# Performance work log

Measured on AMD Instinct MI355X. Metric: run time of the kernel, lower is better.

Reference implementation:

```python
import jax, jax.numpy as jnp
import numpy as np

B, N, D, H = 8, 1024, 768, 12
HD = D // H
SCALE = HD ** -0.5

def setup_inputs() -> dict:
    key = jax.random.key(0)
    k1, k2, k3, k4 = jax.random.split(key, 4)
    x = jax.random.normal(k1, (B, N, D), dtype=jnp.float32)
    weight = jax.random.uniform(k2, (B, N), dtype=jnp.float32)
    W_qkv = jax.random.normal(k3, (D, 3 * D), dtype=jnp.float32) * (D ** -0.5)
    W_msa = jax.random.normal(k4, (D, D), dtype=jnp.float32) * (D ** -0.5)
    b_msa = jnp.zeros((D,), dtype=jnp.float32)
    return {"x": x, "weight": weight, "W_qkv": W_qkv, "W_msa": W_msa, "b_msa": b_msa}

def reference(x, weight, W_qkv, W_msa, b_msa):
    # QKV projection (no bias), then elementwise per-token gate
    qkv = jnp.einsum('bnd,de->bne', x, W_qkv)          # [B,N,3D]
    qkv = weight[:, :, None] * qkv
    qkv = qkv.reshape(B, N, 3, H, HD).transpose(2, 0, 3, 1, 4)  # [3,B,H,N,hd]
    q, k, v = qkv[0], qkv[1], qkv[2]
    A = jnp.einsum('bhnd,bhmd->bhnm', q, k) * SCALE    # [B,H,N,N]
    A = jax.nn.softmax(A, axis=-1)
    out = jnp.einsum('bhnm,bhmd->bhnd', A, v)          # [B,H,N,hd]
    out = out.transpose(0, 2, 1, 3).reshape(B, N, D)
    return jnp.einsum('bnd,de->bne', out, W_msa) + b_msa
```

## Files before the change

### kernel.cpp

```cpp
#include <hip/hip_runtime.h>
#include <hip/hip_bf16.h>


typedef __attribute__((ext_vector_type(8))) short bf8;
typedef __attribute__((ext_vector_type(4))) float f4;

#define QSCALE 0.1803368801111204f
#define MFMA16 __builtin_amdgcn_mfma_f32_16x16x32_bf16

static __device__ __forceinline__ short bf16_of(float f) {
    union { float f; unsigned u; } a; a.f = f;
    unsigned r = a.u + 0x7FFFu + ((a.u >> 16) & 1u);
    return (short)(r >> 16);
}

static __device__ __forceinline__ unsigned bfpk(float lo, float hi) {
    float2 t; t.x = lo; t.y = hi;
    __hip_bfloat162 b = __float22bfloat162_rn(t);
    union { __hip_bfloat162 b; unsigned u; } c; c.b = b;
    return c.u;
}

static __device__ __forceinline__ void async16(const short* g, short* l) {
    __builtin_amdgcn_global_load_lds(
        (const __attribute__((address_space(1))) void*)g,
        (__attribute__((address_space(3))) void*)l, 16, 0, 0);
}

static __device__ __forceinline__ void transpose64(
        const float* __restrict__ w, short* __restrict__ wt,
        int K, int E, int k0, int e0, int tid, short (*t)[65]) {
#pragma unroll
    for (int p = 0; p < 16; ++p) {
        int idx = p * 256 + tid;
        int r = idx >> 6, c = idx & 63;
        t[r][c] = bf16_of(w[(k0 + r) * E + e0 + c]);
    }
    __syncthreads();
#pragma unroll
    for (int p = 0; p < 16; ++p) {
        int idx = p * 256 + tid;
        int r = idx >> 6, c = idx & 63;
        wt[(e0 + r) * K + k0 + c] = t[c][r];
    }
}

__global__ __launch_bounds__(256) void k_prep(
        const float* __restrict__ x, const float* __restrict__ gate,
        short* __restrict__ xb,
        const float* __restrict__ Wqkv, short* __restrict__ wtq,
        const float* __restrict__ Wmsa, short* __restrict__ wtm) {
    __shared__ short t[64][65];
    const int bid = blockIdx.x, tid = threadIdx.x;
    if (bid < 3072) {
        int i = bid * 256 + tid;
        const float g = gate[i / 96];
        const f4* sp = (const f4*)x;
        f4 a = sp[2 * i], b = sp[2 * i + 1];
        union { bf8 v; short h[8]; } o;
        o.h[0] = bf16_of(a[0] * g); o.h[1] = bf16_of(a[1] * g);
        o.h[2] = bf16_of(a[2] * g); o.h[3] = bf16_of(a[3] * g);
        o.h[4] = bf16_of(b[0] * g); o.h[5] = bf16_of(b[1] * g);
        o.h[6] = bf16_of(b[2] * g); o.h[7] = bf16_of(b[3] * g);
        ((bf8*)xb)[i] = o.v;
    } else if (bid < 3504) {
        int tt = bid - 3072;
        transpose64(Wqkv, wtq, 768, 2304, (tt / 36) * 64, (tt % 36) * 64, tid, t);
    } else {
        int tt = bid - 3504;
        transpose64(Wmsa, wtm, 768, 768, (tt / 12) * 64, (tt % 12) * 64, tid, t);
    }
}

__global__ __launch_bounds__(256, 2) void k_gemm_qkv(
        const short* __restrict__ xb, const short* __restrict__ wtq,
        short* __restrict__ qb, short* __restrict__ kb, short* __restrict__ vt) {
    __shared__ short lds[34816];
    const int tid = threadIdx.x, lane = tid & 63;
    const int l16 = lane & 15, quad = lane >> 4, rx = l16 & 7;
    const int wm = tid >> 6;

    const int wg = blockIdx.x;
    const int swz = (wg & 7) * 128 + (wg >> 3);
    const int mI = swz >> 4, nI = swz & 15;
    const int m0 = mI * 128, n0 = nI * 144;

    const short* gA = xb + m0 * 768;
    const short* gB = wtq + n0 * 768;

    auto stageA = [&](int buf, int k0) {
        short* base = lds + buf * 17408;
#pragma unroll
        for (int j = 0; j < 4; ++j) {
            int p = j * 256 + tid, row = p >> 3;
            int gc = (p & 7) ^ (row & 7);
            async16(gA + row * 768 + k0 + gc * 8, base + p * 8);
        }
    };
    auto stageB = [&](int buf, int k0) {
        short* base = lds + buf * 17408 + 8192;
#pragma unroll
        for (int j = 0; j < 4; ++j) {
            int p = j * 256 + tid, row = p >> 3;
            int gc = (p & 7) ^ (row & 7);
            async16(gB + row * 768 + k0 + gc * 8, base + p * 8);
        }
        if (tid < 128) {
            int p = 1024 + tid, row = p >> 3;
            int gc = (p & 7) ^ (row & 7);
            async16(gB + row * 768 + k0 + gc * 8, base + p * 8);
        }
    };

    auto rdA = [&](const short* base, int mf, int ks) {
        return *(const bf8*)(base + (wm * 32 + mf * 16 + l16) * 64 +
                             (((ks * 4 + quad) ^ rx) << 3));
    };
    auto rdB = [&](const short* base, int nf, int ks) {
        return *(const bf8*)(base + 8192 + (nf * 16 + l16) * 64 +
                             (((ks * 4 + quad) ^ rx) << 3));
    };

    f4 z = {0.f, 0.f, 0.f, 0.f};
    f4 acc[2][9];
#pragma unroll
    for (int mf = 0; mf < 2; ++mf)
#pragma unroll
        for (int nf = 0; nf < 9; ++nf) acc[mf][nf] = z;

    stageA(0, 0); stageB(0, 0);
    asm volatile("s_waitcnt vmcnt(0)" ::: "memory");
    __builtin_amdgcn_s_barrier();

#pragma unroll 2
    for (int t = 0; t < 12; ++t) {
        const short* cur = lds + (t & 1) * 17408;
        bf8 af[2][2];
        af[0][0] = rdA(cur, 0, 0); af[0][1] = rdA(cur, 0, 1);
        af[1][0] = rdA(cur, 1, 0); af[1][1] = rdA(cur, 1, 1);
        bf8 bfr[5][2];
#pragma unroll
        for (int nf = 0; nf < 5; ++nf) { bfr[nf][0] = rdB(cur, nf, 0); bfr[nf][1] = rdB(cur, nf, 1); }
        if (t < 11) stageA((t + 1) & 1, (t + 1) * 64);
        __builtin_amdgcn_s_setprio(1);
#pragma unroll
        for (int mf = 0; mf < 2; ++mf)
#pragma unroll
            for (int nf = 0; nf < 5; ++nf) {
                acc[mf][nf] = MFMA16(af[mf][0], bfr[nf][0], acc[mf][nf], 0, 0, 0);
                acc[mf][nf] = MFMA16(af[mf][1], bfr[nf][1], acc[mf][nf], 0, 0, 0);
            }
        __builtin_amdgcn_s_setprio(0);
        bf8 bfh[4][2];
#pragma unroll
        for (int nf = 0; nf < 4; ++nf) { bfh[nf][0] = rdB(cur, nf + 5, 0); bfh[nf][1] = rdB(cur, nf + 5, 1); }
        if (t < 11) stageB((t + 1) & 1, (t + 1) * 64);
        __builtin_amdgcn_s_setprio(1);
#pragma unroll
        for (int mf = 0; mf < 2; ++mf)
#pragma unroll
            for (int nf = 0; nf < 4; ++nf) {
                acc[mf][nf + 5] = MFMA16(af[mf][0], bfh[nf][0], acc[mf][nf + 5], 0, 0, 0);
                acc[mf][nf + 5] = MFMA16(af[mf][1], bfh[nf][1], acc[mf][nf + 5], 0, 0, 0);
            }
        __builtin_amdgcn_s_setprio(0);
        asm volatile("s_waitcnt vmcnt(0)" ::: "memory");
        __builtin_amdgcn_s_barrier();
    }

    const int bI = m0 >> 10, nn0 = m0 & 1023;
#pragma unroll
    for (int nf = 0; nf < 9; ++nf) {
        const int ct = n0 + nf * 16;
        if (ct < 1536) {
            const int which = (ct >= 768) ? 1 : 0;
            const int h = (ct - which * 768) >> 6;
            const int hd = (ct & 63) + l16;
            short* dst = (which ? kb : qb) + (bI * 12 + h) * 65536 + hd;
#pragma unroll
            for (int mf = 0; mf < 2; ++mf)
#pragma unroll
                for (int r = 0; r < 4; ++r) {
                    const int nn = nn0 + wm * 32 + mf * 16 + quad * 4 + r;
                    const float val = acc[mf][nf][r];
                    dst[nn * 64] = bf16_of(which ? val : val * QSCALE);
                }
        }
    }
    const int vlo = (n0 >= 1536) ? n0 : 1536;
    const int vcnt = n0 + 144 - vlo;
    const int npass = (vcnt > 0) ? vcnt / 48 : 0;
    for (int p = 0; p < npass; ++p) {
        __syncthreads();
        const int c0 = vlo + p * 48;
#pragma unroll
        for (int nf = 0; nf < 9; ++nf) {
            const int ct = n0 + nf * 16;
            if (ct >= c0 && ct < c0 + 48) {
                const int lcol = ct - c0 + l16;
#pragma unroll
                for (int mf = 0; mf < 2; ++mf)
#pragma unroll
                    for (int r = 0; r < 4; ++r) {
                        const int row = wm * 32 + mf * 16 + quad * 4 + r;
                        lds[lcol * 136 + row] = bf16_of(acc[mf][nf][r]);
                    }
            }
        }
        __syncthreads();
        const int vg0 = c0 - 1536;
#pragma unroll
        for (int u = 0; u < 3; ++u) {
            const int idx = u * 256 + tid;
            const int lc = idx >> 4, ck = idx & 15;
            const int vg = vg0 + lc;
            const int h = vg >> 6, hd = vg & 63;
            bf8 vv = *(const bf8*)(lds + lc * 136 + ck * 8);
            *(bf8*)(vt + ((bI * 12 + h) * 64 + hd) * 1024 + nn0 + ck * 8) = vv;
        }
    }
}

__global__ __launch_bounds__(256, 2) void k_gemm_final(
        const short* __restrict__ attn, const short* __restrict__ wtm,
        const float* __restrict__ bias, float* __restrict__ out) {
    __shared__ short lds[28672];
    const int tid = threadIdx.x, lane = tid & 63;
    const int l16 = lane & 15, quad = lane >> 4, rx = l16 & 7;
    const int wm = tid >> 6;

    const int wg = blockIdx.x;
    const int swz = (wg & 7) * 64 + (wg >> 3);
    const int mI = swz >> 3, nI = swz & 7;
    const int m0 = mI * 128, n0 = nI * 96;

    const short* gA = attn + m0 * 768;
    const short* gB = wtm + n0 * 768;

    auto stageA = [&](int buf, int k0) {
        short* base = lds + buf * 14336;
#pragma unroll
        for (int j = 0; j < 4; ++j) {
            int p = j * 256 + tid, row = p >> 3;
            int gc = (p & 7) ^ (row & 7);
            async16(gA + row * 768 + k0 + gc * 8, base + p * 8);
        }
    };
    auto stageB = [&](int buf, int k0) {
        short* base = lds + buf * 14336 + 8192;
#pragma unroll
        for (int j = 0; j < 3; ++j) {
            int p = j * 256 + tid, row = p >> 3;
            int gc = (p & 7) ^ (row & 7);
            async16(gB + row * 768 + k0 + gc * 8, base + p * 8);
        }
    };
    auto rdA = [&](const short* base, int mf, int ks) {
        return *(const bf8*)(base + (wm * 32 + mf * 16 + l16) * 64 +
                             (((ks * 4 + quad) ^ rx) << 3));
    };
    auto rdB = [&](const short* base, int nf, int ks) {
        return *(const bf8*)(base + 8192 + (nf * 16 + l16) * 64 +
                             (((ks * 4 + quad) ^ rx) << 3));
    };

    f4 z = {0.f, 0.f, 0.f, 0.f};
    f4 acc[2][6];
#pragma unroll
    for (int mf = 0; mf < 2; ++mf)
#pragma unroll
        for (int nf = 0; nf < 6; ++nf) acc[mf][nf] = z;

    stageA(0, 0); stageB(0, 0);
    asm volatile("s_waitcnt vmcnt(0)" ::: "memory");
    __builtin_amdgcn_s_barrier();

#pragma unroll 2
    for (int t = 0; t < 12; ++t) {
        const short* cur = lds + (t & 1) * 14336;
        bf8 af[2][2];
        af[0][0] = rdA(cur, 0, 0); af[0][1] = rdA(cur, 0, 1);
        af[1][0] = rdA(cur, 1, 0); af[1][1] = rdA(cur, 1, 1);
        bf8 bfr[3][2];
#pragma unroll
        for (int nf = 0; nf < 3; ++nf) { bfr[nf][0] = rdB(cur, nf, 0); bfr[nf][1] = rdB(cur, nf, 1); }
        if (t < 11) stageA((t + 1) & 1, (t + 1) * 64);
        __builtin_amdgcn_s_setprio(1);
#pragma unroll
        for (int mf = 0; mf < 2; ++mf)
#pragma unroll
            for (int nf = 0; nf < 3; ++nf) {
                acc[mf][nf] = MFMA16(af[mf][0], bfr[nf][0], acc[mf][nf], 0, 0, 0);
                acc[mf][nf] = MFMA16(af[mf][1], bfr[nf][1], acc[mf][nf], 0, 0, 0);
            }
        __builtin_amdgcn_s_setprio(0);
        bf8 bfh[3][2];
#pragma unroll
        for (int nf = 0; nf < 3; ++nf) { bfh[nf][0] = rdB(cur, nf + 3, 0); bfh[nf][1] = rdB(cur, nf + 3, 1); }
        if (t < 11) stageB((t + 1) & 1, (t + 1) * 64);
        __builtin_amdgcn_s_setprio(1);
#pragma unroll
        for (int mf = 0; mf < 2; ++mf)
#pragma unroll
            for (int nf = 0; nf < 3; ++nf) {
                acc[mf][nf + 3] = MFMA16(af[mf][0], bfh[nf][0], acc[mf][nf + 3], 0, 0, 0);
                acc[mf][nf + 3] = MFMA16(af[mf][1], bfh[nf][1], acc[mf][nf + 3], 0, 0, 0);
            }
        __builtin_amdgcn_s_setprio(0);
        asm volatile("s_waitcnt vmcnt(0)" ::: "memory");
        __builtin_amdgcn_s_barrier();
    }

#pragma unroll
    for (int nf = 0; nf < 6; ++nf) {
        const int e = n0 + nf * 16 + l16;
        const float bv = bias[e];
#pragma unroll
        for (int mf = 0; mf < 2; ++mf)
#pragma unroll
            for (int r = 0; r < 4; ++r) {
                const int row = m0 + wm * 32 + mf * 16 + quad * 4 + r;
                out[row * 768 + e] = acc[mf][nf][r] + bv;
            }
    }
}

__global__ __launch_bounds__(256, 3) void k_attn(const short* __restrict__ qb,
                                                 const short* __restrict__ kb,
                                                 const short* __restrict__ vt,
                                                 short* __restrict__ attn) {
    __shared__ short Ks[2][4096];
    __shared__ short Vs[2][4096];
    const int tid = threadIdx.x, wave = tid >> 6, lane = tid & 63;
    const int l16 = lane & 15, quad = lane >> 4;
    const int bh = blockIdx.x;
    const int b = bh / 12, h = bh - b * 12;
    const int m_base = blockIdx.y * 128 + wave * 32;
    const short* qh = qb + bh * 65536;
    const short* kh = kb + bh * 65536;
    const short* vh = vt + bh * 65536;

    const int rA = ((l16 >> 2) << 3) + (l16 & 3);
    const int fK = (((rA >> 3) & 1) << 2) + (rA & 3);
    const int sK = (quad ^ fK) * 8;
    const int oAlo = rA * 64 + sK;
    const int oAhi = rA * 64 + (sK ^ 32);
    const int oBlo = oAlo + 256, oBhi = oAhi + 256;
    const int fV = (((l16 >> 3) & 1) << 2) + (l16 & 3);
    const int oV = l16 * 64 + ((quad ^ fV) * 8);

    const short* qp0 = qh + (m_base + l16) * 64 + quad * 8;
    bf8 qf00 = *(const bf8*)(qp0);
    bf8 qf01 = *(const bf8*)(qp0 + 32);
    const short* qp1 = qp0 + 16 * 64;
    bf8 qf10 = *(const bf8*)(qp1);
    bf8 qf11 = *(const bf8*)(qp1 + 32);

    union { bf8 v; short h[8]; } onef;
#pragma unroll
    for (int i = 0; i < 8; ++i) onef.h[i] = (short)0x3F80;

    f4 z = {0.f, 0.f, 0.f, 0.f};
    f4 acc0[4] = {z, z, z, z};
    f4 acc1[4] = {z, z, z, z};
    f4 accl0 = z, accl1 = z;

    auto stage = [&](int buf, int j0) {
#pragma unroll
        for (int j = 0; j < 2; ++j) {
            int idx = j * 256 + tid;
            int row = idx >> 3;
            int fr = (((row >> 3) & 1) << 2) + (row & 3);
            int gc = (idx & 7) ^ fr;
            async16(kh + (j0 + row) * 64 + gc * 8, Ks[buf] + idx * 8);
            async16(vh + row * 1024 + j0 + gc * 8, Vs[buf] + idx * 8);
        }
    };

    stage(0, 0);
    int cur = 0;
    for (int it = 0; it < 16; ++it) {
        __builtin_amdgcn_s_waitcnt(0);
        __syncthreads();
        if (it + 1 < 16) stage(cur ^ 1, (it + 1) * 64);
        const short* Kc = Ks[cur];
        const short* Vc = Vs[cur];

#pragma unroll
        for (int jj = 0; jj < 64; jj += 32) {
            const short* kjj = Kc + jj * 64;
            bf8 kAlo = *(const bf8*)(kjj + oAlo);
            bf8 kAhi = *(const bf8*)(kjj + oAhi);
            bf8 kBlo = *(const bf8*)(kjj + oBlo);
            bf8 kBhi = *(const bf8*)(kjj + oBhi);
            bf8 vf0 = *(const bf8*)(Vc + 0 * 1024 + (oV ^ (jj ? 32 : 0)));
            bf8 vf1 = *(const bf8*)(Vc + 1 * 1024 + (oV ^ (jj ? 32 : 0)));
            bf8 vf2 = *(const bf8*)(Vc + 2 * 1024 + (oV ^ (jj ? 32 : 0)));
            bf8 vf3 = *(const bf8*)(Vc + 3 * 1024 + (oV ^ (jj ? 32 : 0)));

            {
                f4 sA = z, sB = z;
                __builtin_amdgcn_s_setprio(1);
                sA = MFMA16(kAlo, qf00, sA, 0, 0, 0);
                sA = MFMA16(kAhi, qf01, sA, 0, 0, 0);
                sB = MFMA16(kBlo, qf00, sB, 0, 0, 0);
                sB = MFMA16(kBhi, qf01, sB, 0, 0, 0);
                __builtin_amdgcn_s_setprio(0);
                float a0 = __builtin_amdgcn_exp2f(sA[0]);
                float a1 = __builtin_amdgcn_exp2f(sA[1]);
                float a2 = __builtin_amdgcn_exp2f(sA[2]);
                float a3 = __builtin_amdgcn_exp2f(sA[3]);
                float b0 = __builtin_amdgcn_exp2f(sB[0]);
                float b1 = __builtin_amdgcn_exp2f(sB[1]);
                float b2 = __builtin_amdgcn_exp2f(sB[2]);
                float b3 = __builtin_amdgcn_exp2f(sB[3]);
                union { bf8 v; unsigned u[4]; } p;
                p.u[0] = bfpk(a0, a1); p.u[1] = bfpk(a2, a3);
                p.u[2] = bfpk(b0, b1); p.u[3] = bfpk(b2, b3);
                __builtin_amdgcn_s_setprio(1);
                accl0 = MFMA16(onef.v, p.v, accl0, 0, 0, 0);
                acc0[0] = MFMA16(vf0, p.v, acc0[0], 0, 0, 0);
                acc0[1] = MFMA16(vf1, p.v, acc0[1], 0, 0, 0);
                acc0[2] = MFMA16(vf2, p.v, acc0[2], 0, 0, 0);
                acc0[3] = MFMA16(vf3, p.v, acc0[3], 0, 0, 0);
                __builtin_amdgcn_s_setprio(0);
            }
            {
                f4 sA = z, sB = z;
                __builtin_amdgcn_s_setprio(1);
                sA = MFMA16(kAlo, qf10, sA, 0, 0, 0);
                sA = MFMA16(kAhi, qf11, sA, 0, 0, 0);
                sB = MFMA16(kBlo, qf10, sB, 0, 0, 0);
                sB = MFMA16(kBhi, qf11, sB, 0, 0, 0);
                __builtin_amdgcn_s_setprio(0);
                float a0 = __builtin_amdgcn_exp2f(sA[0]);
                float a1 = __builtin_amdgcn_exp2f(sA[1]);
                float a2 = __builtin_amdgcn_exp2f(sA[2]);
                float a3 = __builtin_amdgcn_exp2f(sA[3]);
                float b0 = __builtin_amdgcn_exp2f(sB[0]);
                float b1 = __builtin_amdgcn_exp2f(sB[1]);
                float b2 = __builtin_amdgcn_exp2f(sB[2]);
                float b3 = __builtin_amdgcn_exp2f(sB[3]);
                union { bf8 v; unsigned u[4]; } p;
                p.u[0] = bfpk(a0, a1); p.u[1] = bfpk(a2, a3);
                p.u[2] = bfpk(b0, b1); p.u[3] = bfpk(b2, b3);
                __builtin_amdgcn_s_setprio(1);
                accl1 = MFMA16(onef.v, p.v, accl1, 0, 0, 0);
                acc1[0] = MFMA16(vf0, p.v, acc1[0], 0, 0, 0);
                acc1[1] = MFMA16(vf1, p.v, acc1[1], 0, 0, 0);
                acc1[2] = MFMA16(vf2, p.v, acc1[2], 0, 0, 0);
                acc1[3] = MFMA16(vf3, p.v, acc1[3], 0, 0, 0);
                __builtin_amdgcn_s_setprio(0);
            }
        }
        cur ^= 1;
    }

    const float inv0 = 1.f / accl0[0];
    const float inv1 = 1.f / accl1[0];
    const int row0 = (b << 10) + m_base + l16;
    short* op0 = attn + row0 * 768 + h * 64 + quad * 4;
    short* op1 = op0 + 16 * 768;
#pragma unroll
    for (int dt = 0; dt < 4; ++dt)
#pragma unroll
        for (int r = 0; r < 4; ++r) {
            op0[dt * 16 + r] = bf16_of(acc0[dt][r] * inv0);
            op1[dt * 16 + r] = bf16_of(acc1[dt][r] * inv1);
        }
}

extern "C" void kernel_launch(void* const* d_in, const int* in_sizes, int n_in,
                              void* d_out, int out_size, void* d_ws, size_t ws_size,
                              hipStream_t stream) {
    const float* x    = (const float*)d_in[0];
    const float* gate = (const float*)d_in[1];
    const float* Wqkv = (const float*)d_in[2];
    const float* Wmsa = (const float*)d_in[3];
    const float* bmsa = (const float*)d_in[4];
    float* out = (float*)d_out;

    char* ws = (char*)d_ws;
    short* xb  = (short*)(ws);
    short* wtq = (short*)(ws + 12582912);
    short* wtm = (short*)(ws + 16121856);
    short* qb  = (short*)(ws + 17301504);
    short* kb  = (short*)(ws + 29884416);
    short* vt  = (short*)(ws + 42467328);
    short* attn = xb;

    k_prep<<<3648, 256, 0, stream>>>(x, gate, xb, Wqkv, wtq, Wmsa, wtm);
    k_gemm_qkv<<<1024, 256, 0, stream>>>(xb, wtq, qb, kb, vt);
    k_attn<<<dim3(96, 8), 256, 0, stream>>>(qb, kb, vt, attn);
    k_gemm_final<<<512, 256, 0, stream>>>(attn, wtm, bmsa, out);
}
```

Baseline: 179.0 us.

## Deepen QKV GEMM pipeline to four stages with K=32 tiles and partial waits

Reworks the QKV projection GEMM from a double-buffered K=64 loop into a four-buffer K=32 pipeline that prefetches three tiles ahead. Waits use partial vmcnt counts per wave so the next tile's loads can stay in flight, which is meant to hide global-to-LDS latency better. The LDS swizzle is changed to suit 32-wide rows. The trade-off is twice as many barriers and iterations, and a redundant duplicated store line added in k_prep.

```diff
diff --git a/kernel.cpp b/kernel.cpp
--- a/kernel.cpp
+++ b/kernel.cpp
@@ -61,6 +61,7 @@
         o.h[0] = bf16_of(a[0] * g); o.h[1] = bf16_of(a[1] * g);
         o.h[2] = bf16_of(a[2] * g); o.h[3] = bf16_of(a[3] * g);
         o.h[4] = bf16_of(b[0] * g); o.h[5] = bf16_of(b[1] * g);
+        o.h[6] = bf16_of(b[2] * g); o.h[7] = bf16_of(b[7 - 4] * g);
         o.h[6] = bf16_of(b[2] * g); o.h[7] = bf16_of(b[3] * g);
         ((bf8*)xb)[i] = o.v;
     } else if (bid < 3504) {
@@ -77,7 +78,7 @@
         short* __restrict__ qb, short* __restrict__ kb, short* __restrict__ vt) {
     __shared__ short lds[34816];
     const int tid = threadIdx.x, lane = tid & 63;
-    const int l16 = lane & 15, quad = lane >> 4, rx = l16 & 7;
+    const int l16 = lane & 15, quad = lane >> 4;
     const int wm = tid >> 6;
 
     const int wg = blockIdx.x;
@@ -88,37 +89,36 @@
     const short* gA = xb + m0 * 768;
     const short* gB = wtq + n0 * 768;
 
-    auto stageA = [&](int buf, int k0) {
-        short* base = lds + buf * 17408;
-#pragma unroll
-        for (int j = 0; j < 4; ++j) {
-            int p = j * 256 + tid, row = p >> 3;
-            int gc = (p & 7) ^ (row & 7);
+    auto stage = [&](int buf, int k0) {
+        short* base = lds + buf * 8704;
+#pragma unroll
+        for (int j = 0; j < 2; ++j) {
+            int p = j * 256 + tid, row = p >> 2;
+            int gc = (p & 3) ^ ((row >> 1) & 3);
             async16(gA + row * 768 + k0 + gc * 8, base + p * 8);
         }
-    };
-    auto stageB = [&](int buf, int k0) {
-        short* base = lds + buf * 17408 + 8192;
-#pragma unroll
-        for (int j = 0; j < 4; ++j) {
-            int p = j * 256 + tid, row = p >> 3;
-            int gc = (p & 7) ^ (row & 7);
-            async16(gB + row * 768 + k0 + gc * 8, base + p * 8);
-        }
-        if (tid < 128) {
-            int p = 1024 + tid, row = p >> 3;
-            int gc = (p & 7) ^ (row & 7);
-            async16(gB + row * 768 + k0 + gc * 8, base + p * 8);
-        }
-    };
-
-    auto rdA = [&](const short* base, int mf, int ks) {
-        return *(const bf8*)(base + (wm * 32 + mf * 16 + l16) * 64 +
-                             (((ks * 4 + quad) ^ rx) << 3));
-    };
-    auto rdB = [&](const short* base, int nf, int ks) {
-        return *(const bf8*)(base + 8192 + (nf * 16 + l16) * 64 +
-                             (((ks * 4 + quad) ^ rx) << 3));
+#pragma unroll
+        for (int j = 0; j < 2; ++j) {
+            int p = j * 256 + tid, row = p >> 2;
+            int gc = (p & 3) ^ ((row >> 1) & 3);
+            async16(gB + row * 768 + k0 + gc * 8, base + 4096 + p * 8);
+        }
+        if (tid < 64) {
+            int p = 512 + tid, row = p >> 2;
+            int gc = (p & 3) ^ ((row >> 1) & 3);
+            async16(gB + row * 768 + k0 + gc * 8, base + 4096 + p * 8);
+        }
+    };
+
+    auto rdA = [&](const short* base, int mf) {
+        int row = wm * 32 + mf * 16 + l16;
+        return *(const bf8*)(base + row * 32 +
+                             ((quad ^ ((row >> 1) & 3)) << 3));
+    };
+    auto rdB = [&](const short* base, int nf) {
+        int row = nf * 16 + l16;
+        return *(const bf8*)(base + 4096 + row * 32 +
+                             ((quad ^ ((row >> 1) & 3)) << 3));
     };
 
     f4 z = {0.f, 0.f, 0.f, 0.f};
@@ -128,44 +128,37 @@
 #pragma unroll
         for (int nf = 0; nf < 9; ++nf) acc[mf][nf] = z;
 
-    stageA(0, 0); stageB(0, 0);
-    asm volatile("s_waitcnt vmcnt(0)" ::: "memory");
+    stage(0, 0); stage(1, 32); stage(2, 64);
+    if (wm == 0) asm volatile("s_waitcnt vmcnt(10)" ::: "memory");
+    else         asm volatile("s_waitcnt vmcnt(8)" ::: "memory");
     __builtin_amdgcn_s_barrier();
 
-#pragma unroll 2
-    for (int t = 0; t < 12; ++t) {
-        const short* cur = lds + (t & 1) * 17408;
-        bf8 af[2][2];
-        af[0][0] = rdA(cur, 0, 0); af[0][1] = rdA(cur, 0, 1);
-        af[1][0] = rdA(cur, 1, 0); af[1][1] = rdA(cur, 1, 1);
-        bf8 bfr[5][2];
-#pragma unroll
-        for (int nf = 0; nf < 5; ++nf) { bfr[nf][0] = rdB(cur, nf, 0); bfr[nf][1] = rdB(cur, nf, 1); }
-        if (t < 11) stageA((t + 1) & 1, (t + 1) * 64);
+#pragma unroll 4
+    for (int t = 0; t < 24; ++t) {
+        const short* cur = lds + (t & 3) * 8704;
+        bf8 af0 = rdA(cur, 0);
+        bf8 af1 = rdA(cur, 1);
+        bf8 bfr[9];
+#pragma unroll
+        for (int nf = 0; nf < 9; ++nf) bfr[nf] = rdB(cur, nf);
+        if (t < 21) stage((t + 3) & 3, (t + 3) * 32);
         __builtin_amdgcn_s_setprio(1);
 #pragma unroll
-        for (int mf = 0; mf < 2; ++mf)
-#pragma unroll
-            for (int nf = 0; nf < 5; ++nf) {
-                acc[mf][nf] = MFMA16(af[mf][0], bfr[nf][0], acc[mf][nf], 0, 0, 0);
-                acc[mf][nf] = MFMA16(af[mf][1], bfr[nf][1], acc[mf][nf], 0, 0, 0);
-            }
+        for (int nf = 0; nf < 9; ++nf) {
+            acc[0][nf] = MFMA16(af0, bfr[nf], acc[0][nf], 0, 0, 0);
+            acc[1][nf] = MFMA16(af1, bfr[nf], acc[1][nf], 0, 0, 0);
+        }
         __builtin_amdgcn_s_setprio(0);
-        bf8 bfh[4][2];
-#pragma unroll
-        for (int nf = 0; nf < 4; ++nf) { bfh[nf][0] = rdB(cur, nf + 5, 0); bfh[nf][1] = rdB(cur, nf + 5, 1); }
-        if (t < 11) stageB((t + 1) & 1, (t + 1) * 64);
-        __builtin_amdgcn_s_setprio(1);
-#pragma unroll
-        for (int mf = 0; mf < 2; ++mf)
-#pragma unroll
-            for (int nf = 0; nf < 4; ++nf) {
-                acc[mf][nf + 5] = MFMA16(af[mf][0], bfh[nf][0], acc[mf][nf + 5], 0, 0, 0);
-                acc[mf][nf + 5] = MFMA16(af[mf][1], bfh[nf][1], acc[mf][nf + 5], 0, 0, 0);
-            }
-        __builtin_amdgcn_s_setprio(0);
-        asm volatile("s_waitcnt vmcnt(0)" ::: "memory");
-        __builtin_amdgcn_s_barrier();
+        if (t < 21) {
+            if (wm == 0) asm volatile("s_waitcnt vmcnt(10)" ::: "memory");
+            else         asm volatile("s_waitcnt vmcnt(8)" ::: "memory");
+        } else if (t == 21) {
+            if (wm == 0) asm volatile("s_waitcnt vmcnt(5)" ::: "memory");
+            else         asm volatile("s_waitcnt vmcnt(4)" ::: "memory");
+        } else if (t == 22) {
+            asm volatile("s_waitcnt vmcnt(0)" ::: "memory");
+        }
+        if (t < 23) __builtin_amdgcn_s_barrier();
     }
 
     const int bI = m0 >> 10, nn0 = m0 & 1023;
```

After: 172.0 us. 3.9% less time.
